# Performance work log

Hardware: AMD Instinct MI355X
Metric: run time of the kernel (lower is better)

## Reference

```python
import jax, jax.numpy as jnp
import numpy as np

EPS = 1e-05  # module eps (both LayerNorm and mask-count denominator)


def setup_inputs() -> dict:
    key = jax.random.key(0)
    ks = jax.random.split(key, 6)
    b, m, n, dm, dh, dp = 1, 256, 384, 256, 32, 128
    x = jax.random.normal(ks[0], (b, m, n, dm), jnp.float32)
    mask = jnp.ones((b, m, n), dtype=bool)
    ln_g = jnp.ones((dm,), jnp.float32)
    ln_b = jnp.zeros((dm,), jnp.float32)
    wl = jax.random.normal(ks[1], (dm, dh), jnp.float32) * 0.02
    bl = jnp.zeros((dh,), jnp.float32)
    wr = jax.random.normal(ks[2], (dm, dh), jnp.float32) * 0.02
    br = jnp.zeros((dh,), jnp.float32)
    wo = jax.random.normal(ks[3], (dh * dh, dp), jnp.float32) * 0.02
    bo = jnp.zeros((dp,), jnp.float32)
    return dict(x=x, mask=mask, ln_g=ln_g, ln_b=ln_b, wl=wl, bl=bl,
                wr=wr, br=br, wo=wo, bo=bo)


def reference(x, mask, ln_g, ln_b, wl, bl, wr, br, wo, bo):
    # x: (b, m, i, dim_msa); mask: (b, m, i)
    mu = jnp.mean(x, axis=-1, keepdims=True)
    var = jnp.var(x, axis=-1, keepdims=True)
    xn = (x - mu) / jnp.sqrt(var + EPS) * ln_g + ln_b

    mf = mask.astype(x.dtype)  # (b, m, i)
    # mask_i * mask_j on the outer product == masking left and right separately
    left = (xn @ wl + bl) * mf[..., None]   # (b, m, i, dh)
    right = (xn @ wr + br) * mf[..., None]  # (b, m, j, dh)

    # sum over MSA depth m without materializing the (b,m,i,j,c,d) tensor
    outer = jnp.einsum('bmic,bmjd->bijcd', left, right)  # (b, i, j, dh, dh)
    b_, n_ = outer.shape[0], outer.shape[1]
    out = outer.reshape(b_, n_, n_, -1) @ wo + bo  # (b, i, j, dim_pairwise)

    # normalize by pairwise mask count (matches masked branch of the module)
    count = jnp.einsum('bmi,bmj->bij', mf, mf)[..., None]  # (b, i, j, 1)
    return out / (count + EPS)
```

## Files before the change

kernel.cpp:

```cpp
#include <hip/hip_runtime.h>
#include <hip/hip_bf16.h>

#define EPS 1e-5f
#define MM 256
#define NN 384
#define DM 256
#define DH 32
#define DP 128
#define NIC (NN*DH)

typedef __attribute__((ext_vector_type(8))) short short8;
typedef __attribute__((ext_vector_type(4))) float floatx4;

__device__ __forceinline__ void load16_to_lds(const void* gptr, void* lptr) {
    __builtin_amdgcn_global_load_lds(
        (const __attribute__((address_space(1))) void*)gptr,
        (__attribute__((address_space(3))) void*)lptr,
        16, 0, 0);
}

__device__ __forceinline__ unsigned short f2bf_bits(float f) {
    __hip_bfloat16 h = __float2bfloat16(f);
    union { __hip_bfloat16 h; unsigned short u; } cvt;
    cvt.h = h;
    return cvt.u;
}

__global__ __launch_bounds__(256) void kprep(
    const float* __restrict__ wo, unsigned short* __restrict__ woT2,
    const float* __restrict__ wl, const float* __restrict__ bl,
    const float* __restrict__ wr, const float* __restrict__ br,
    unsigned short* __restrict__ WbT, float* __restrict__ bias,
    const int* __restrict__ mask, unsigned int* __restrict__ pack)
{
    __shared__ float ts[64*129];
    const int bid = blockIdx.x;
    const int t   = threadIdx.x;

    if (bid < 16) {
        const int s  = bid >> 2;
        const int dg = bid & 3;
        #pragma unroll
        for (int g = 0; g < 32; g++) {
            int idx = g*256 + t;
            int row = idx >> 7, p = idx & 127;
            int ci = row >> 3, di = row & 7;
            int cd = (s*8 + ci)*32 + dg*8 + di;
            ts[row*129 + p] = wo[(size_t)cd*DP + p];
        }
        __syncthreads();
        int p = t >> 1, half = t & 1;
        #pragma unroll
        for (int dq = 0; dq < 4; dq++) {
            int di = half*4 + dq;
            #pragma unroll
            for (int cq = 0; cq < 2; cq++) {
                ushort4 u;
                u.x = f2bf_bits(ts[((cq*4+0)*8 + di)*129 + p]);
                u.y = f2bf_bits(ts[((cq*4+1)*8 + di)*129 + p]);
                u.z = f2bf_bits(ts[((cq*4+2)*8 + di)*129 + p]);
                u.w = f2bf_bits(ts[((cq*4+3)*8 + di)*129 + p]);
                *(ushort4*)&woT2[(size_t)p*1024 + s*256 + dg*64 + di*8 + cq*4] = u;
            }
        }
    } else if (bid < 80) {
        const int c = bid - 16, k = t;
        float v = (c < DH) ? wl[k*DH + c] : wr[k*DH + (c - DH)];
        WbT[c*256 + k] = f2bf_bits(v);
        if (c == 0 && k < 64) bias[k] = (k < DH) ? bl[k] : br[k - DH];
    } else {
        int id = (bid - 80)*256 + t;
        int i = id % NN, tw = id / NN;
        unsigned int wbits = 0;
        #pragma unroll
        for (int b = 0; b < 32; b++)
            wbits |= (mask[(tw*32 + b)*NN + i] != 0 ? 1u : 0u) << b;
        pack[i*8 + tw] = wbits;
    }
}

__global__ __launch_bounds__(256) void k2_count(
    const unsigned int* __restrict__ pack, float* __restrict__ cinv)
{
    int id = blockIdx.x * 256 + threadIdx.x;
    int i = id / NN, j = id % NN;
    int s = 0;
    #pragma unroll
    for (int tw = 0; tw < 8; tw++)
        s += __popc(pack[i*8 + tw] & pack[j*8 + tw]);
    cinv[id] = 1.0f / ((float)s + EPS);
}

__global__ __launch_bounds__(256, 2) void k1_lnproj(
    const float* __restrict__ x, const int* __restrict__ mask,
    const float* __restrict__ ln_g, const float* __restrict__ ln_b,
    const unsigned short* __restrict__ WbTg, const float* __restrict__ bias,
    unsigned short* __restrict__ Lb, unsigned short* __restrict__ Rb)
{
    __shared__ unsigned short xns[64*264];
    __shared__ float mfs[64];

    const int i  = blockIdx.x;
    const int mc = blockIdx.y;
    const int t = threadIdx.x;
    const int l = t & 63, w = t >> 6;
    const int lc = l & 15, quad = l >> 4;
    const int sub = l >> 4, lc4 = l & 15;

    float4 gk[4], bk[4];
    #pragma unroll
    for (int g = 0; g < 4; g++) {
        gk[g] = *(const float4*)&ln_g[g*64 + lc4*4];
        bk[g] = *(const float4*)&ln_b[g*64 + lc4*4];
    }

    float4 v[4][4];
    #pragma unroll
    for (int rr = 0; rr < 4; rr++) {
        int mlocal = w*16 + rr*4 + sub;
        int m = mc*64 + mlocal;
        const float4* xr = (const float4*)&x[((size_t)m*NN + i)*DM];
        #pragma unroll
        for (int g = 0; g < 4; g++)
            v[rr][g] = xr[g*16 + lc4];
    }

    #pragma unroll
    for (int rr = 0; rr < 4; rr++) {
        int mlocal = w*16 + rr*4 + sub;
        int m = mc*64 + mlocal;
        float s = 0.f, s2 = 0.f;
        #pragma unroll
        for (int g = 0; g < 4; g++) {
            float4 vg = v[rr][g];
            s  += vg.x + vg.y + vg.z + vg.w;
            s2 += vg.x*vg.x + vg.y*vg.y + vg.z*vg.z + vg.w*vg.w;
        }
        #pragma unroll
        for (int off = 1; off < 16; off <<= 1) {
            s  += __shfl_xor(s,  off, 64);
            s2 += __shfl_xor(s2, off, 64);
        }
        float mu   = s * (1.0f/DM);
        float var  = s2 * (1.0f/DM) - mu*mu;
        float rstd = rsqrtf(var + EPS);
        #pragma unroll
        for (int g = 0; g < 4; g++) {
            float4 vg = v[rr][g];
            ushort4 u;
            u.x = f2bf_bits((vg.x - mu)*rstd*gk[g].x + bk[g].x);
            u.y = f2bf_bits((vg.y - mu)*rstd*gk[g].y + bk[g].y);
            u.z = f2bf_bits((vg.z - mu)*rstd*gk[g].z + bk[g].z);
            u.w = f2bf_bits((vg.w - mu)*rstd*gk[g].w + bk[g].w);
            *(ushort4*)&xns[mlocal*264 + g*64 + lc4*4] = u;
        }
        if (lc4 == 0) mfs[mlocal] = (mask[(size_t)m*NN + i] != 0) ? 1.0f : 0.0f;
    }
    __syncthreads();

    floatx4 acc[4];
    #pragma unroll
    for (int nt = 0; nt < 4; nt++) acc[nt] = (floatx4){0.f,0.f,0.f,0.f};
    #pragma unroll
    for (int ks = 0; ks < 8; ks++) {
        short8 af = *(const short8*)&xns[(w*16 + lc)*264 + ks*32 + quad*8];
        #pragma unroll
        for (int nt = 0; nt < 4; nt++) {
            short8 bf = *(const short8*)&WbTg[(nt*16 + lc)*256 + ks*32 + quad*8];
            acc[nt] = __builtin_amdgcn_mfma_f32_16x16x32_bf16(af, bf, acc[nt], 0, 0, 0);
        }
    }
    __syncthreads();

    unsigned short* tr = xns;
    #pragma unroll
    for (int nt = 0; nt < 4; nt++) {
        int c = nt*16 + lc;
        float bv = bias[c];
        #pragma unroll
        for (int rg = 0; rg < 4; rg++) {
            int mlocal = w*16 + quad*4 + rg;
            tr[c*72 + mlocal] = f2bf_bits((acc[nt][rg] + bv) * mfs[mlocal]);
        }
    }
    __syncthreads();

    {
        int c = t >> 2, seg = t & 3;
        unsigned short* dst = (c < DH)
            ? &Lb[((size_t)(i*DH + c))*MM + mc*64 + seg*16]
            : &Rb[((size_t)(i*DH + (c - DH)))*MM + mc*64 + seg*16];
        #pragma unroll
        for (int q = 0; q < 4; q++)
            *(ushort4*)&dst[q*4] = *(ushort4*)&tr[c*72 + seg*16 + q*4];
    }
}

__global__ __launch_bounds__(512, 2) void k3f_gemm(
    const unsigned short* __restrict__ Lb,
    const unsigned short* __restrict__ Rb,
    const unsigned short* __restrict__ woT2,
    const float* __restrict__ bo, const float* __restrict__ cinv,
    float* __restrict__ out)
{
    __shared__ short smem[32768];
    const int t = threadIdx.x;
    const int l = t & 63, w = t >> 6;
    const int wx = w & 3, wy = w >> 2;
    const int lc = l & 15, quad = l >> 4;

    int bid = blockIdx.x;
    int xcd = bid & 7;
    int local = bid >> 3;
    int bx = local / 6;
    int by = xcd * 6 + (local % 6);

    const size_t arow0 = (size_t)bx * 256;
    const size_t brow0 = (size_t)by * 256;

    const int pos0 = t, pos1 = 512 + t;
    const int line0 = pos0 >> 3, c0 = (pos0 & 7) ^ (line0 & 7);
    const int r0 = line0*2 + (c0 >> 2), k00 = (c0 & 3) * 8;
    const int line1 = pos1 >> 3, c1 = (pos1 & 7) ^ (line1 & 7);
    const int r1 = line1*2 + (c1 >> 2), k01 = (c1 & 3) * 8;

    const unsigned short* srcA0 = Lb + (arow0 + r0)*MM + k00;
    const unsigned short* srcA1 = Lb + (arow0 + r1)*MM + k01;
    const unsigned short* srcB0 = Rb + (brow0 + r0)*MM + k00;
    const unsigned short* srcB1 = Rb + (brow0 + r1)*MM + k01;

    floatx4 acc[8][4];
    #pragma unroll
    for (int a = 0; a < 8; a++)
        #pragma unroll
        for (int b = 0; b < 4; b++) acc[a][b] = (floatx4){0.f,0.f,0.f,0.f};

#define STAGE(bsel, step) do {                                           \
        char* sb = (char*)smem + (bsel)*32768;                           \
        load16_to_lds(srcA0 + (step)*32, sb + pos0*16);                  \
        load16_to_lds(srcA1 + (step)*32, sb + pos1*16);                  \
        load16_to_lds(srcB0 + (step)*32, sb + 16384 + pos0*16);          \
        load16_to_lds(srcB1 + (step)*32, sb + 16384 + pos1*16);          \
    } while (0)

    STAGE(0, 0);
    STAGE(1, 1);
    #pragma unroll
    for (int tstep = 0; tstep < 8; tstep++) {
        if (tstep < 7) asm volatile("s_waitcnt vmcnt(4)" ::: "memory");
        else           asm volatile("s_waitcnt vmcnt(0)" ::: "memory");
        __builtin_amdgcn_s_barrier();
        __builtin_amdgcn_sched_barrier(0);
        const char* Ab = (const char*)smem + (tstep & 1)*32768;
        const char* Bb = Ab + 16384;
        short8 bfr[4];
        #pragma unroll
        for (int nt = 0; nt < 4; nt++) {
            int r = wx*64 + nt*16 + lc;
            int li = r >> 1, cc = ((r & 1)*4 + quad) ^ (li & 7);
            bfr[nt] = *(const short8*)(Bb + li*128 + cc*16);
        }
        __builtin_amdgcn_s_setprio(1);
        #pragma unroll
        for (int mt = 0; mt < 8; mt++) {
            int r = wy*128 + mt*16 + lc;
            int li = r >> 1, cc = ((r & 1)*4 + quad) ^ (li & 7);
            short8 af = *(const short8*)(Ab + li*128 + cc*16);
            #pragma unroll
            for (int nt = 0; nt < 4; nt++)
                acc[mt][nt] = __builtin_amdgcn_mfma_f32_16x16x32_bf16(
                    af, bfr[nt], acc[mt][nt], 0, 0, 0);
        }
        __builtin_amdgcn_s_setprio(0);
        __builtin_amdgcn_s_barrier();
        __builtin_amdgcn_sched_barrier(0);
        if (tstep + 2 < 8) STAGE(tstep & 1, tstep + 2);
    }
#undef STAGE

    short* gp = smem;
    const int prow = w*16 + lc;
    floatx4 acc2[4];
    #pragma unroll
    for (int a = 0; a < 4; a++) acc2[a] = (floatx4){0.f,0.f,0.f,0.f};

    #pragma unroll
    for (int s = 0; s < 4; s++) {
        short8 b2r[8];
        #pragma unroll
        for (int ks = 0; ks < 8; ks++)
            b2r[ks] = *(const short8*)&woT2[(size_t)prow*1024 + s*256 + ks*32 + quad*8];

        if ((quad >> 1) == (s & 1)) {
            #pragma unroll
            for (int mmi = 0; mmi < 4; mmi++) {
                const int mt = (s >> 1) + mmi*2;
                #pragma unroll
                for (int nt = 0; nt < 4; nt++) {
                    int pair = (wy*4 + (mt >> 1))*8 + (wx*2 + (nt >> 1));
                    int d = (nt & 1)*16 + lc;
                    int kk = d*8 + (quad & 1)*4;
                    ushort4 u;
                    u.x = f2bf_bits(acc[mt][nt][0]);
                    u.y = f2bf_bits(acc[mt][nt][1]);
                    u.z = f2bf_bits(acc[mt][nt][2]);
                    u.w = f2bf_bits(acc[mt][nt][3]);
                    *(ushort4*)&gp[pair*264 + kk] = u;
                }
            }
        }
        __syncthreads();

        __builtin_amdgcn_s_setprio(1);
        #pragma unroll
        for (int ks = 0; ks < 8; ks++) {
            #pragma unroll
            for (int mt2 = 0; mt2 < 4; mt2++) {
                short8 a2 = *(const short8*)&gp[(mt2*16 + lc)*264 + ks*32 + quad*8];
                acc2[mt2] = __builtin_amdgcn_mfma_f32_16x16x32_bf16(
                    a2, b2r[ks], acc2[mt2], 0, 0, 0);
            }
        }
        __builtin_amdgcn_s_setprio(0);
        __syncthreads();
    }

    const float bv = bo[prow];
    #pragma unroll
    for (int mt2 = 0; mt2 < 4; mt2++) {
        #pragma unroll
        for (int rg = 0; rg < 4; rg++) {
            int pair = mt2*16 + quad*4 + rg;
            int i = bx*8 + (pair >> 3);
            int j = by*8 + (pair & 7);
            out[((size_t)(i*NN + j))*DP + prow] =
                (acc2[mt2][rg] + bv) * cinv[i*NN + j];
        }
    }
}

extern "C" void kernel_launch(void* const* d_in, const int* in_sizes, int n_in,
                              void* d_out, int out_size, void* d_ws, size_t ws_size,
                              hipStream_t stream)
{
    const float* x    = (const float*)d_in[0];
    const int*   mask = (const int*)d_in[1];
    const float* ln_g = (const float*)d_in[2];
    const float* ln_b = (const float*)d_in[3];
    const float* wl   = (const float*)d_in[4];
    const float* bl   = (const float*)d_in[5];
    const float* wr   = (const float*)d_in[6];
    const float* br   = (const float*)d_in[7];
    const float* wo   = (const float*)d_in[8];
    const float* bo   = (const float*)d_in[9];
    float* out = (float*)d_out;

    char* ws = (char*)d_ws;
    size_t off = 0;
    unsigned short* Lb   = (unsigned short*)(ws + off); off += (size_t)NIC*MM*2;
    unsigned short* Rb   = (unsigned short*)(ws + off); off += (size_t)NIC*MM*2;
    unsigned short* woT2 = (unsigned short*)(ws + off); off += (size_t)DP*1024*2;
    unsigned short* WbTg = (unsigned short*)(ws + off); off += (size_t)64*256*2;
    float*          bias = (float*)(ws + off);          off += 64*4;
    float*          cinv = (float*)(ws + off);          off += (size_t)NN*NN*4;
    unsigned int*   pack = (unsigned int*)Lb;

    kprep<<<92, 256, 0, stream>>>(wo, woT2, wl, bl, wr, br, WbTg, bias, mask, pack);
    k2_count<<<(NN*NN)/256, 256, 0, stream>>>(pack, cinv);
    k1_lnproj<<<dim3(NN, MM/64), 256, 0, stream>>>(x, mask, ln_g, ln_b, WbTg, bias, Lb, Rb);
    k3f_gemm<<<2304, 512, 0, stream>>>(Lb, Rb, woT2, bo, cinv, out);
}
```

Before: 349.2 us.

## Switch bf16 MFMA path to fp16 and split main GEMM into four launches

Replaces bf16 storage and MFMA instructions with fp16 equivalents across the LN projection, outer-product GEMM and output projection. It also splits the single 2304-block GEMM launch into four launches with a block offset. fp16 gives more mantissa precision but less dynamic range, and the split adds launch overhead and tail effects. The motive for the split is unclear; it may be a scheduling experiment.

```diff
diff --git a/kernel.cpp b/kernel.cpp
--- a/kernel.cpp
+++ b/kernel.cpp
@@ -9,7 +9,7 @@
 #define DP 128
 #define NIC (NN*DH)
 
-typedef __attribute__((ext_vector_type(8))) short short8;
+typedef __attribute__((ext_vector_type(8))) _Float16 half8;
 typedef __attribute__((ext_vector_type(4))) float floatx4;
 
 __device__ __forceinline__ void load16_to_lds(const void* gptr, void* lptr) {
@@ -19,9 +19,9 @@
         16, 0, 0);
 }
 
-__device__ __forceinline__ unsigned short f2bf_bits(float f) {
-    __hip_bfloat16 h = __float2bfloat16(f);
-    union { __hip_bfloat16 h; unsigned short u; } cvt;
+__device__ __forceinline__ unsigned short f2h_bits(float f) {
+    _Float16 h = (_Float16)f;
+    union { _Float16 h; unsigned short u; } cvt;
     cvt.h = h;
     return cvt.u;
 }
@@ -56,17 +56,17 @@
             #pragma unroll
             for (int cq = 0; cq < 2; cq++) {
                 ushort4 u;
-                u.x = f2bf_bits(ts[((cq*4+0)*8 + di)*129 + p]);
-                u.y = f2bf_bits(ts[((cq*4+1)*8 + di)*129 + p]);
-                u.z = f2bf_bits(ts[((cq*4+2)*8 + di)*129 + p]);
-                u.w = f2bf_bits(ts[((cq*4+3)*8 + di)*129 + p]);
+                u.x = f2h_bits(ts[((cq*4+0)*8 + di)*129 + p]);
+                u.y = f2h_bits(ts[((cq*4+1)*8 + di)*129 + p]);
+                u.z = f2h_bits(ts[((cq*4+2)*8 + di)*129 + p]);
+                u.w = f2h_bits(ts[((cq*4+3)*8 + di)*129 + p]);
                 *(ushort4*)&woT2[(size_t)p*1024 + s*256 + dg*64 + di*8 + cq*4] = u;
             }
         }
     } else if (bid < 80) {
         const int c = bid - 16, k = t;
         float v = (c < DH) ? wl[k*DH + c] : wr[k*DH + (c - DH)];
-        WbT[c*256 + k] = f2bf_bits(v);
+        WbT[c*256 + k] = f2h_bits(v);
         if (c == 0 && k < 64) bias[k] = (k < DH) ? bl[k] : br[k - DH];
     } else {
         int id = (bid - 80)*256 + t;
@@ -148,10 +148,10 @@
         for (int g = 0; g < 4; g++) {
             float4 vg = v[rr][g];
             ushort4 u;
-            u.x = f2bf_bits((vg.x - mu)*rstd*gk[g].x + bk[g].x);
-            u.y = f2bf_bits((vg.y - mu)*rstd*gk[g].y + bk[g].y);
-            u.z = f2bf_bits((vg.z - mu)*rstd*gk[g].z + bk[g].z);
-            u.w = f2bf_bits((vg.w - mu)*rstd*gk[g].w + bk[g].w);
+            u.x = f2h_bits((vg.x - mu)*rstd*gk[g].x + bk[g].x);
+            u.y = f2h_bits((vg.y - mu)*rstd*gk[g].y + bk[g].y);
+            u.z = f2h_bits((vg.z - mu)*rstd*gk[g].z + bk[g].z);
+            u.w = f2h_bits((vg.w - mu)*rstd*gk[g].w + bk[g].w);
             *(ushort4*)&xns[mlocal*264 + g*64 + lc4*4] = u;
         }
         if (lc4 == 0) mfs[mlocal] = (mask[(size_t)m*NN + i] != 0) ? 1.0f : 0.0f;
@@ -163,11 +163,11 @@
     for (int nt = 0; nt < 4; nt++) acc[nt] = (floatx4){0.f,0.f,0.f,0.f};
     #pragma unroll
     for (int ks = 0; ks < 8; ks++) {
-        short8 af = *(const short8*)&xns[(w*16 + lc)*264 + ks*32 + quad*8];
+        half8 af = *(const half8*)&xns[(w*16 + lc)*264 + ks*32 + quad*8];
         #pragma unroll
         for (int nt = 0; nt < 4; nt++) {
-            short8 bf = *(const short8*)&WbTg[(nt*16 + lc)*256 + ks*32 + quad*8];
-            acc[nt] = __builtin_amdgcn_mfma_f32_16x16x32_bf16(af, bf, acc[nt], 0, 0, 0);
+            half8 bf = *(const half8*)&WbTg[(nt*16 + lc)*256 + ks*32 + quad*8];
+            acc[nt] = __builtin_amdgcn_mfma_f32_16x16x32_f16(af, bf, acc[nt], 0, 0, 0);
         }
     }
     __syncthreads();
@@ -180,7 +180,7 @@
         #pragma unroll
         for (int rg = 0; rg < 4; rg++) {
             int mlocal = w*16 + quad*4 + rg;
-            tr[c*72 + mlocal] = f2bf_bits((acc[nt][rg] + bv) * mfs[mlocal]);
+            tr[c*72 + mlocal] = f2h_bits((acc[nt][rg] + bv) * mfs[mlocal]);
         }
     }
     __syncthreads();
@@ -201,7 +201,7 @@
     const unsigned short* __restrict__ Rb,
     const unsigned short* __restrict__ woT2,
     const float* __restrict__ bo, const float* __restrict__ cinv,
-    float* __restrict__ out)
+    float* __restrict__ out, int bofs)
 {
     __shared__ short smem[32768];
     const int t = threadIdx.x;
@@ -209,7 +209,7 @@
     const int wx = w & 3, wy = w >> 2;
     const int lc = l & 15, quad = l >> 4;
 
-    int bid = blockIdx.x;
+    int bid = blockIdx.x + bofs;
     int xcd = bid & 7;
     int local = bid >> 3;
     int bx = local / 6;
@@ -253,22 +253,22 @@
         __builtin_amdgcn_sched_barrier(0);
         const char* Ab = (const char*)smem + (tstep & 1)*32768;
         const char* Bb = Ab + 16384;
-        short8 bfr[4];
+        half8 bfr[4];
         #pragma unroll
         for (int nt = 0; nt < 4; nt++) {
             int r = wx*64 + nt*16 + lc;
             int li = r >> 1, cc = ((r & 1)*4 + quad) ^ (li & 7);
-            bfr[nt] = *(const short8*)(Bb + li*128 + cc*16);
+            bfr[nt] = *(const half8*)(Bb + li*128 + cc*16);
         }
         __builtin_amdgcn_s_setprio(1);
         #pragma unroll
         for (int mt = 0; mt < 8; mt++) {
             int r = wy*128 + mt*16 + lc;
             int li = r >> 1, cc = ((r & 1)*4 + quad) ^ (li & 7);
-            short8 af = *(const short8*)(Ab + li*128 + cc*16);
+            half8 af = *(const half8*)(Ab + li*128 + cc*16);
             #pragma unroll
             for (int nt = 0; nt < 4; nt++)
-                acc[mt][nt] = __builtin_amdgcn_mfma_f32_16x16x32_bf16(
+                acc[mt][nt] = __builtin_amdgcn_mfma_f32_16x16x32_f16(
                     af, bfr[nt], acc[mt][nt], 0, 0, 0);
         }
         __builtin_amdgcn_s_setprio(0);
@@ -286,10 +286,10 @@
 
     #pragma unroll
     for (int s = 0; s < 4; s++) {
-        short8 b2r[8];
+        half8 b2r[8];
         #pragma unroll
         for (int ks = 0; ks < 8; ks++)
-            b2r[ks] = *(const short8*)&woT2[(size_t)prow*1024 + s*256 + ks*32 + quad*8];
+            b2r[ks] = *(const half8*)&woT2[(size_t)prow*1024 + s*256 + ks*32 + quad*8];
 
         if ((quad >> 1) == (s & 1)) {
             #pragma unroll
@@ -301,10 +301,10 @@
                     int d = (nt & 1)*16 + lc;
                     int kk = d*8 + (quad & 1)*4;
                     ushort4 u;
-                    u.x = f2bf_bits(acc[mt][nt][0]);
-                    u.y = f2bf_bits(acc[mt][nt][1]);
-                    u.z = f2bf_bits(acc[mt][nt][2]);
-                    u.w = f2bf_bits(acc[mt][nt][3]);
+                    u.x = f2h_bits(acc[mt][nt][0]);
+                    u.y = f2h_bits(acc[mt][nt][1]);
+                    u.z = f2h_bits(acc[mt][nt][2]);
+                    u.w = f2h_bits(acc[mt][nt][3]);
                     *(ushort4*)&gp[pair*264 + kk] = u;
                 }
             }
@@ -316,8 +316,8 @@
         for (int ks = 0; ks < 8; ks++) {
             #pragma unroll
             for (int mt2 = 0; mt2 < 4; mt2++) {
-                short8 a2 = *(const short8*)&gp[(mt2*16 + lc)*264 + ks*32 + quad*8];
-                acc2[mt2] = __builtin_amdgcn_mfma_f32_16x16x32_bf16(
+                half8 a2 = *(const half8*)&gp[(mt2*16 + lc)*264 + ks*32 + quad*8];
+                acc2[mt2] = __builtin_amdgcn_mfma_f32_16x16x32_f16(
                     a2, b2r[ks], acc2[mt2], 0, 0, 0);
             }
         }
@@ -368,5 +368,8 @@
     kprep<<<92, 256, 0, stream>>>(wo, woT2, wl, bl, wr, br, WbTg, bias, mask, pack);
     k2_count<<<(NN*NN)/256, 256, 0, stream>>>(pack, cinv);
     k1_lnproj<<<dim3(NN, MM/64), 256, 0, stream>>>(x, mask, ln_g, ln_b, WbTg, bias, Lb, Rb);
-    k3f_gemm<<<2304, 512, 0, stream>>>(Lb, Rb, woT2, bo, cinv, out);
-}
+    k3f_gemm<<< 512, 512, 0, stream>>>(Lb, Rb, woT2, bo, cinv, out, 0);
+    k3f_gemm<<< 512, 512, 0, stream>>>(Lb, Rb, woT2, bo, cinv, out, 512);
+    k3f_gemm<<< 512, 512, 0, stream>>>(Lb, Rb, woT2, bo, cinv, out, 1024);
+    k3f_gemm<<< 768, 512, 0, stream>>>(Lb, Rb, woT2, bo, cinv, out, 1536);
+}
```

Result: slower. 363.4 us (+4.1%).
